# Optimization experiments

Hardware: AMD Instinct MI355X
Metric: run time of the kernel (lower is better)

## Reference

```python
import jax, jax.numpy as jnp
from jax import lax
import numpy as np

S = 3600  # spatial_size from scn.InputLayer
B = 1     # batch
P = 200000
NEG = jnp.float32(-1e30)


def setup_inputs() -> dict:
    key = jax.random.key(0)
    ks = jax.random.split(key, 10)
    coords = jax.random.randint(ks[0], (P, 2), 0, S, dtype=jnp.int32)
    features = jax.random.normal(ks[1], (P, 1), jnp.float32)
    w1 = jax.random.normal(ks[2], (5, 5, 1, 10), jnp.float32) * 0.2
    w2 = jax.random.normal(ks[3], (5, 5, 10, 64), jnp.float32) * 0.06
    w3 = jax.random.normal(ks[4], (5, 5, 64, 128), jnp.float32) * 0.025
    w4 = jax.random.normal(ks[5], (5, 5, 128, 256), jnp.float32) * 0.018
    fc1_w = jax.random.normal(ks[6], (256 * 9 * 9, 32), jnp.float32) * 0.01
    fc1_b = jax.random.normal(ks[7], (32,), jnp.float32) * 0.01
    fc2_w = jax.random.normal(ks[8], (32, 5), jnp.float32) * 0.1
    fc2_b = jax.random.normal(ks[9], (5,), jnp.float32) * 0.01
    return dict(coords=coords, features=features, w1=w1, w2=w2, w3=w3, w4=w4,
                fc1_w=fc1_w, fc1_b=fc1_b, fc2_w=fc2_w, fc2_b=fc2_b)


def _subm_conv(x, mask, w):
    # Submanifold conv == dense SAME conv on zero-filled grid, output kept
    # only at active sites (inactive inputs are exactly zero by construction).
    y = lax.conv_general_dilated(x, w, (1, 1), 'SAME',
                                 dimension_numbers=('NHWC', 'HWIO', 'NHWC'))
    return y * mask


def _sparse_maxpool(x, mask, k):
    # scn.MaxPooling: max over ACTIVE sites in each window; output site is
    # active iff any input site in the window is active, else feature = 0.
    neg = jnp.where(mask > 0, x, NEG)
    y = lax.reduce_window(neg, NEG, lax.max, (1, k, k, 1), (1, k, k, 1), 'VALID')
    new_mask = lax.reduce_window(mask, jnp.float32(0), lax.max,
                                 (1, k, k, 1), (1, k, k, 1), 'VALID')
    return jnp.where(new_mask > 0, y, 0.0), new_mask


def reference(coords, features, w1, w2, w3, w4, fc1_w, fc1_b, fc2_w, fc2_b):
    # scn.InputLayer: scatter sparse (coord, feature) pairs onto the grid
    x = jnp.zeros((B, S, S, 1), jnp.float32).at[0, coords[:, 0], coords[:, 1], :].add(features)
    mask = jnp.zeros((B, S, S, 1), jnp.float32).at[0, coords[:, 0], coords[:, 1], :].set(1.0)

    x = jax.nn.elu(_subm_conv(x, mask, w1))
    x, mask = _sparse_maxpool(x, mask, 5)   # 3600 -> 720
    x = jax.nn.elu(_subm_conv(x, mask, w2))
    x, mask = _sparse_maxpool(x, mask, 5)   # 720 -> 144
    x = jax.nn.elu(_subm_conv(x, mask, w3))
    x, mask = _sparse_maxpool(x, mask, 4)   # 144 -> 36
    x = jax.nn.elu(_subm_conv(x, mask, w4))
    x, mask = _sparse_maxpool(x, mask, 4)   # 36 -> 9

    # SparseToDense -> (B, 256, 9, 9), then view(-1, 256*9*9) in NCHW order
    h = x.transpose(0, 3, 1, 2).reshape(B, 256 * 9 * 9)
    h = jax.nn.elu(h @ fc1_w + fc1_b)
    logits = h @ fc2_w + fc2_b
    return jax.nn.softmax(logits, axis=1)
```

## Files before the change

kernel.cpp:

```cpp
#include <hip/hip_runtime.h>
#include <math.h>

#define S0 3600
#define S1 720
#define S2 144
#define S3 36
#define S4 9
#define NEGF (-1e30f)

static constexpr size_t OFF_X0  = 0;
static constexpr size_t OFF_M0B = (size_t)S0 * S0 * 4;
static constexpr size_t OFF_H1  = OFF_M0B + 1620000;
static constexpr size_t OFF_CNT = OFF_H1 + 128;
static constexpr size_t OFF_Y1H = OFF_CNT + 32;
static constexpr size_t OFF_M1  = OFF_Y1H + (size_t)S1 * S1 * 16 * 2;
static constexpr size_t OFF_M2  = 1330000;
static constexpr size_t OFF_Y3  = OFF_M2 + 20736;
static constexpr size_t OFF_M3  = OFF_Y3 + (size_t)S3 * S3 * 128 * 4;
static constexpr size_t OFF_Y4  = OFF_M3 + 1296;
static constexpr size_t OFF_Y2H = 80000000;
static constexpr size_t OFF_W2H = 84000000;
static constexpr size_t OFF_W3H = 84200000;
static constexpr size_t OFF_W4H = 84700000;

typedef __attribute__((ext_vector_type(8))) short bf16x8;
typedef __attribute__((ext_vector_type(4))) float f32x4;

__device__ __forceinline__ float eluf(float x) { return x > 0.f ? x : expm1f(x); }
__device__ __forceinline__ unsigned short f2bf(float f) {
    unsigned u = __float_as_uint(f);
    unsigned r = u + 0x7FFFu + ((u >> 16) & 1u);
    return (unsigned short)(r >> 16);
}
__device__ __forceinline__ float bf2f(unsigned short h) {
    return __uint_as_float((unsigned)h << 16);
}

__global__ __launch_bounds__(256) void k_zero(const int* __restrict__ coords,
                                              float* __restrict__ x0, int P) {
    int i = blockIdx.x * 256 + threadIdx.x;
    if (i >= P) return;
    x0[coords[2 * i] * S0 + coords[2 * i + 1]] = 0.f;
}

__global__ __launch_bounds__(256) void k_scatter(const int* __restrict__ coords,
                                                 const float* __restrict__ feats,
                                                 float* __restrict__ x0,
                                                 unsigned* __restrict__ m0b, int P) {
    int i = blockIdx.x * 256 + threadIdx.x;
    if (i >= P) return;
    int r = coords[2 * i], c = coords[2 * i + 1];
    int idx = r * S0 + c;
    atomicAdd(&x0[idx], feats[i]);
    atomicOr(&m0b[idx >> 5], 1u << (idx & 31));
}

__global__ __launch_bounds__(256) void k_l1c(const float* __restrict__ x0,
                                             const unsigned* __restrict__ m0b,
                                             const float* __restrict__ w1,
                                             const float* __restrict__ w2,
                                             const float* __restrict__ w3,
                                             const float* __restrict__ w4,
                                             unsigned short* __restrict__ y1h,
                                             unsigned char* __restrict__ m1,
                                             unsigned short* __restrict__ w2h,
                                             unsigned short* __restrict__ w3h,
                                             unsigned short* __restrict__ w4h) {
    int b = blockIdx.x;
    int tid = threadIdx.x;
    if (b >= 2025) {
        int blk = b - 2025;
        if (blk < 13) {
            int t = blk * 256 + tid;
            int s = t >> 8, rem = t & 255;
            int nt = rem >> 6, lane = rem & 63;
            int quad = lane >> 4, n = lane & 15;
            int tap = 2 * s + (quad >> 1);
#pragma unroll
            for (int j = 0; j < 8; j++) {
                int ci = (quad & 1) * 8 + j;
                float v = 0.f;
                if (tap < 25 && ci < 10) v = w2[(tap * 10 + ci) * 64 + nt * 16 + n];
                w2h[(size_t)t * 8 + j] = f2bf(v);
            }
        } else if (blk < 113) {
            int t = (blk - 13) * 256 + tid;
            int s = t >> 9, rem = t & 511;
            int nt = rem >> 6, lane = rem & 63;
            int quad = lane >> 4, n = lane & 15;
            int t5 = s >> 1, cib = s & 1;
#pragma unroll
            for (int j = 0; j < 8; j++) {
                int ci = cib * 32 + quad * 8 + j;
                float v = w3[(size_t)(t5 * 64 + ci) * 128 + nt * 16 + n];
                w3h[(size_t)t * 8 + j] = f2bf(v);
            }
        } else {
            int t = (blk - 113) * 256 + tid;
            int s = t >> 10, rem = t & 1023;
            int nt = rem >> 6, lane = rem & 63;
            int quad = lane >> 4, n = lane & 15;
            int t5 = s >> 2, cib = s & 3;
#pragma unroll
            for (int j = 0; j < 8; j++) {
                int ci = cib * 32 + quad * 8 + j;
                float v = w4[(size_t)(t5 * 128 + ci) * 256 + nt * 16 + n];
                w4h[(size_t)t * 8 + j] = f2bf(v);
            }
        }
        return;
    }
    __shared__ float w1s[250];
    if (tid < 250) w1s[tid] = w1[tid];
    __syncthreads();
    int t = b * 256 + tid;
    int pr = t / S1, pc = t % S1;
    int r0 = pr * 5 - 2, c0 = pc * 5 - 2;
    unsigned rows[9];
#pragma unroll
    for (int rr = 0; rr < 9; rr++) {
        unsigned bits = 0;
        int gr = r0 + rr;
        if (gr >= 0 && gr < S0) {
            int cs = c0 < 0 ? 0 : c0;
            int ce = c0 + 8 > S0 - 1 ? S0 - 1 : c0 + 8;
            int span = ce - cs;
            size_t i0 = (size_t)gr * S0 + cs;
            unsigned sh = (unsigned)(i0 & 31);
            unsigned long long two = (unsigned long long)m0b[i0 >> 5] >> sh;
            if ((int)sh + span >= 32)
                two |= (unsigned long long)m0b[(i0 >> 5) + 1] << (32 - sh);
            bits = (unsigned)(two & ((1u << (span + 1)) - 1));
            bits <<= (cs - c0);
        }
        rows[rr] = bits;
    }
    unsigned any25 = 0;
#pragma unroll
    for (int dy = 0; dy < 5; dy++) any25 |= (rows[2 + dy] >> 2) & 0x1Fu;
    uint4* yo = (uint4*)&y1h[(size_t)t * 16];
    if (!any25) {
        yo[0] = make_uint4(0, 0, 0, 0);
        yo[1] = make_uint4(0, 0, 0, 0);
        m1[t] = 0;
        return;
    }
    float2 mx[5];
#pragma unroll
    for (int q = 0; q < 5; q++) mx[q] = make_float2(NEGF, NEGF);
    for (int dy = 0; dy < 5; dy++) {
        unsigned crow = (rows[2 + dy] >> 2) & 0x1Fu;
        while (crow) {
            int dx = __ffs(crow) - 1; crow &= crow - 1;
            float2 acc[5];
#pragma unroll
            for (int q = 0; q < 5; q++) acc[q] = make_float2(0.f, 0.f);
#pragma unroll
            for (int ky = 0; ky < 5; ky++) {
                unsigned nrow = (rows[dy + ky] >> dx) & 0x1Fu;
                size_t rowbase = (size_t)(r0 + dy + ky) * S0 + (c0 + dx);
                while (nrow) {
                    int kx = __ffs(nrow) - 1; nrow &= nrow - 1;
                    float xv = x0[rowbase + kx];
                    const float2* wp = (const float2*)&w1s[(ky * 5 + kx) * 10];
#pragma unroll
                    for (int q = 0; q < 5; q++) {
                        float2 w = wp[q];
                        acc[q].x = fmaf(xv, w.x, acc[q].x);
                        acc[q].y = fmaf(xv, w.y, acc[q].y);
                    }
                }
            }
#pragma unroll
            for (int q = 0; q < 5; q++) {
                mx[q].x = fmaxf(mx[q].x, acc[q].x);
                mx[q].y = fmaxf(mx[q].y, acc[q].y);
            }
        }
    }
    unsigned u[8];
#pragma unroll
    for (int q = 0; q < 5; q++) {
        unsigned short h0 = f2bf(eluf(mx[q].x));
        unsigned short h1 = f2bf(eluf(mx[q].y));
        u[q] = (unsigned)h0 | ((unsigned)h1 << 16);
    }
    u[5] = 0; u[6] = 0; u[7] = 0;
    yo[0] = make_uint4(u[0], u[1], u[2], u[3]);
    yo[1] = make_uint4(u[4], u[5], u[6], u[7]);
    m1[t] = 1;
}

__global__ __launch_bounds__(256, 4) void k_l2(const unsigned short* __restrict__ y1h,
                                               const unsigned char* __restrict__ m1,
                                               const unsigned short* __restrict__ w2h,
                                               unsigned short* __restrict__ y2h,
                                               unsigned char* __restrict__ m2) {
    __shared__ unsigned short winh[240 * 24];
    __shared__ unsigned char sm[196];
    int b = blockIdx.x;
    int bpr = b / 72, bpc = b % 72;
    int r0 = bpr * 10 - 2, c0 = bpc * 10 - 2;
    int tid = threadIdx.x;
    if (tid < 240) {
        uint4 v0 = make_uint4(0, 0, 0, 0), v1 = v0;
        if (tid < 196) {
            int gr = r0 + tid / 14, gc = c0 + tid % 14;
            bool ok = (gr >= 0 && gr < S1 && gc >= 0 && gc < S1);
            sm[tid] = ok ? m1[gr * S1 + gc] : (unsigned char)0;
            if (ok) {
                const uint4* src = (const uint4*)&y1h[(size_t)(gr * S1 + gc) * 16];
                v0 = src[0];
                v1 = src[1];
            }
        }
        uint4* dh = (uint4*)&winh[tid * 24];
        dh[0] = v0;
        dh[1] = v1;
    }
    __syncthreads();
    int wv = tid >> 6;
    int a = wv >> 1, bq = wv & 1;
    int lane = tid & 63, quad = lane >> 4, n = lane & 15;
    int cql = lane & 31, s01l = lane >> 5;
    bool pv = false;
    if (cql < 25)
        pv = sm[(a * 5 + 2 + cql / 5) * 14 + s01l * 5 + 2 + cql % 5] != 0;
    unsigned long long bal = __ballot(pv);
    unsigned mb[2];
    mb[0] = (unsigned)(bal & 0x1FFFFFFull);
    mb[1] = (unsigned)((bal >> 32) & 0x1FFFFFFull);
    const bf16x8* wh8 = (const bf16x8*)w2h;
    const bf16x8* xh8 = (const bf16x8*)winh;
    int oct = quad & 1, qh = quad >> 1;
    int base[2][2];
#pragma unroll
    for (int s01 = 0; s01 < 2; s01++)
#pragma unroll
        for (int mt = 0; mt < 2; mt++) {
            int cell = mt * 16 + n;
            base[s01][mt] = ((a * 5 + cell / 5) * 14 + s01 * 5 + cell % 5) * 3 + oct;
        }
    constexpr int TOFF[26] = {0, 1, 2, 3, 4, 14, 15, 16, 17, 18, 28, 29, 30, 31,
                              32, 42, 43, 44, 45, 46, 56, 57, 58, 59, 60, 70};
    f32x4 acc[2][2][2];
#pragma unroll
    for (int s01 = 0; s01 < 2; s01++)
#pragma unroll
        for (int mt = 0; mt < 2; mt++)
#pragma unroll
            for (int ntl = 0; ntl < 2; ntl++) acc[s01][mt][ntl] = (f32x4){0.f, 0.f, 0.f, 0.f};
#pragma unroll
    for (int s = 0; s < 13; s++) {
        int toff3 = 3 * (qh ? TOFF[2 * s + 1] : TOFF[2 * s]);
        bf16x8 ah[2][2];
#pragma unroll
        for (int s01 = 0; s01 < 2; s01++)
#pragma unroll
            for (int mt = 0; mt < 2; mt++) ah[s01][mt] = xh8[base[s01][mt] + toff3];
#pragma unroll
        for (int ntl = 0; ntl < 2; ntl++) {
            bf16x8 bh = wh8[(s * 4 + bq * 2 + ntl) * 64 + lane];
#pragma unroll
            for (int s01 = 0; s01 < 2; s01++)
#pragma unroll
                for (int mt = 0; mt < 2; mt++)
                    acc[s01][mt][ntl] = __builtin_amdgcn_mfma_f32_16x16x32_bf16(ah[s01][mt], bh, acc[s01][mt][ntl], 0, 0, 0);
        }
    }
#pragma unroll
    for (int s01 = 0; s01 < 2; s01++) {
        int gsite = (bpr * 2 + a) * S2 + bpc * 2 + s01;
#pragma unroll
        for (int ntl = 0; ntl < 2; ntl++) {
            float m = NEGF;
#pragma unroll
            for (int mt = 0; mt < 2; mt++) {
#pragma unroll
                for (int r = 0; r < 4; r++) {
                    int cell = mt * 16 + quad * 4 + r;
                    if (cell < 25 && (mb[s01] & (1u << cell))) m = fmaxf(m, acc[s01][mt][ntl][r]);
                }
            }
            m = fmaxf(m, __shfl_xor(m, 16, 64));
            m = fmaxf(m, __shfl_xor(m, 32, 64));
            if (quad == 0) {
                int nt = bq * 2 + ntl;
                y2h[(size_t)gsite * 64 + nt * 16 + n] = mb[s01] ? f2bf(eluf(m)) : (unsigned short)0;
            }
        }
        if (bq == 0 && lane == 0) m2[gsite] = mb[s01] ? 1 : 0;
    }
}

__global__ __launch_bounds__(256) void k_l3(const unsigned short* __restrict__ y2h,
                                            const unsigned char* __restrict__ m2,
                                            const unsigned short* __restrict__ w3h,
                                            float* __restrict__ y3,
                                            unsigned char* __restrict__ m3) {
    __shared__ uint4 win_h4[144 * 9];
    __shared__ unsigned char sm[64];
    int b = blockIdx.x;
    int pr2 = b / 18, pc2 = b % 18;
    int r0 = pr2 * 8 - 2, c0 = pc2 * 8 - 2;
    int tid = threadIdx.x;
    for (int k = tid; k < 1152; k += 256) {
        int cellk = k >> 3, q = k & 7;
        int gr = r0 + cellk / 12, gc = c0 + cellk % 12;
        uint4 vh = make_uint4(0, 0, 0, 0);
        if (gr >= 0 && gr < S2 && gc >= 0 && gc < S2)
            vh = ((const uint4*)y2h)[(size_t)(gr * S2 + gc) * 8 + q];
        win_h4[cellk * 9 + q] = vh;
    }
    if (tid < 64) sm[tid] = m2[(pr2 * 8 + (tid >> 3)) * S2 + pc2 * 8 + (tid & 7)];
    __syncthreads();
    const bf16x8* winh8 = (const bf16x8*)win_h4;
    const bf16x8* w3h8 = (const bf16x8*)w3h;
    int wv = tid >> 6, lane = tid & 63;
    int quad = lane >> 4, n = lane & 15;
    int cellr = n >> 2, cellc = n & 3;
    f32x4 acc[4][2];
#pragma unroll
    for (int si = 0; si < 4; si++)
#pragma unroll
        for (int ntl = 0; ntl < 2; ntl++) acc[si][ntl] = (f32x4){0.f, 0.f, 0.f, 0.f};
    int bb = (wv * 2) * 64 + lane;
    bf16x8 bh0 = w3h8[bb];
    bf16x8 bh1 = w3h8[bb + 64];
#pragma unroll 2
    for (int s = 0; s < 50; s++) {
        int sp = s + 1 < 50 ? s + 1 : 0;
        int nb = (sp * 8 + wv * 2) * 64 + lane;
        bf16x8 nh0 = w3h8[nb];
        bf16x8 nh1 = w3h8[nb + 64];
        int t5 = s >> 1, cib = s & 1;
        int ky = t5 / 5, kx = t5 % 5;
        int common = ((cellr + ky) * 12 + (cellc + kx)) * 9 + cib * 4 + quad;
#pragma unroll
        for (int si = 0; si < 4; si++) {
            bf16x8 ah = winh8[common + (si >> 1) * 432 + (si & 1) * 36];
            acc[si][0] = __builtin_amdgcn_mfma_f32_16x16x32_bf16(ah, bh0, acc[si][0], 0, 0, 0);
            acc[si][1] = __builtin_amdgcn_mfma_f32_16x16x32_bf16(ah, bh1, acc[si][1], 0, 0, 0);
        }
        bh0 = nh0; bh1 = nh1;
    }
#pragma unroll
    for (int si = 0; si < 4; si++) {
        int srb = (si >> 1) * 4, scb = (si & 1) * 4;
        bool anyv = false;
#pragma unroll
        for (int i = 0; i < 16; i++) anyv |= (sm[(srb + (i >> 2)) * 8 + scb + (i & 3)] != 0);
        int sg = (2 * pr2 + (si >> 1)) * S3 + 2 * pc2 + (si & 1);
#pragma unroll
        for (int ntl = 0; ntl < 2; ntl++) {
            float mv = NEGF;
#pragma unroll
            for (int r = 0; r < 4; r++) {
                int cell = quad * 4 + r;
                if (sm[(srb + (cell >> 2)) * 8 + scb + (cell & 3)]) mv = fmaxf(mv, acc[si][ntl][r]);
            }
            mv = fmaxf(mv, __shfl_xor(mv, 16, 64));
            mv = fmaxf(mv, __shfl_xor(mv, 32, 64));
            if (quad == 0)
                y3[(size_t)sg * 128 + (wv * 2 + ntl) * 16 + n] = anyv ? eluf(mv) : 0.f;
        }
        if (tid == 0) m3[sg] = anyv ? 1 : 0;
    }
}

__global__ __launch_bounds__(1024) void k_l4(const float* __restrict__ y3,
                                             const unsigned char* __restrict__ m3,
                                             const unsigned short* __restrict__ w4h,
                                             float* __restrict__ y4) {
    __shared__ unsigned short winh[1120 * 8];
    __shared__ unsigned char sm[16];
    int p = blockIdx.x;
    int ppr = p / S4, ppc = p % S4;
    int r0 = ppr * 4 - 2, c0 = ppc * 4 - 2;
    int tid = threadIdx.x;
    for (int k = tid; k < 2048; k += 1024) {
        int cellk = k >> 5, q = k & 31;
        int cr = cellk >> 3, cc = cellk & 7;
        int gr = r0 + cr, gc = c0 + cc;
        float4 v = make_float4(0.f, 0.f, 0.f, 0.f);
        if (gr >= 0 && gr < S3 && gc >= 0 && gc < S3)
            v = ((const float4*)y3)[((size_t)gr * S3 + gc) * 32 + q];
        unsigned short h0 = f2bf(v.x), h1 = f2bf(v.y), h2 = f2bf(v.z), h3 = f2bf(v.w);
        unsigned uh0 = (unsigned)h0 | ((unsigned)h1 << 16);
        unsigned uh1 = (unsigned)h2 | ((unsigned)h3 << 16);
        ((uint2*)winh)[cr * 280 + cc * 34 + q] = make_uint2(uh0, uh1);
    }
    if (tid < 16) sm[tid] = m3[(ppr * 4 + (tid >> 2)) * S3 + ppc * 4 + (tid & 3)];
    __syncthreads();
    const bf16x8* winh8 = (const bf16x8*)winh;
    const bf16x8* w4h8 = (const bf16x8*)w4h;
    int wv = tid >> 6, lane = tid & 63;
    int quad = lane >> 4, n = lane & 15;
    int cellr = n >> 2, cellc = n & 3;
    f32x4 acc = {0.f, 0.f, 0.f, 0.f};
    int wb = wv * 64 + lane;
    bf16x8 bha = w4h8[wb];
    bf16x8 bhb = w4h8[1024 + wb];
#pragma unroll 2
    for (int s = 0; s < 100; s++) {
        int sp = s + 2 < 100 ? s + 2 : 0;
        bf16x8 nh = w4h8[sp * 1024 + wb];
        int t5 = s >> 2, cib = s & 3;
        int ky = t5 / 5, kx = t5 % 5;
        int aidx = (cellr + ky) * 140 + (cellc + kx) * 17 + cib * 4 + quad;
        bf16x8 ah = winh8[aidx];
        acc = __builtin_amdgcn_mfma_f32_16x16x32_bf16(ah, bha, acc, 0, 0, 0);
        bha = bhb; bhb = nh;
    }
    bool anyv = false;
#pragma unroll
    for (int i = 0; i < 16; i++) anyv |= (sm[i] != 0);
    float m = NEGF;
#pragma unroll
    for (int r = 0; r < 4; r++) {
        int cell = quad * 4 + r;
        if (sm[cell]) m = fmaxf(m, acc[r]);
    }
    m = fmaxf(m, __shfl_xor(m, 16, 64));
    m = fmaxf(m, __shfl_xor(m, 32, 64));
    if (quad == 0)
        y4[(size_t)p * 256 + wv * 16 + n] = anyv ? eluf(m) : 0.f;
}

__global__ __launch_bounds__(256) void k_fc(const float* __restrict__ y4,
                                            const float* __restrict__ fc1_w,
                                            const float* __restrict__ fc1_b,
                                            const float* __restrict__ fc2_w,
                                            const float* __restrict__ fc2_b,
                                            float* __restrict__ h1,
                                            unsigned* __restrict__ cnt,
                                            float* __restrict__ out) {
    __shared__ float wsum[4][32];
    __shared__ int lastflag;
    __shared__ float hv[32];
    __shared__ float lg[5];
    int t = threadIdx.x;
    int i = blockIdx.x * 256 + t;
    int c = i / 81, rem = i % 81;
    float x = y4[(size_t)rem * 256 + c];
    const float4* wr = (const float4*)&fc1_w[(size_t)i * 32];
    float4 w[8];
#pragma unroll
    for (int q = 0; q < 8; q++) w[q] = wr[q];
    int lane = t & 63, wv = t >> 6;
#pragma unroll
    for (int q = 0; q < 8; q++) {
#pragma unroll
        for (int k = 0; k < 4; k++) {
            float v = x * ((&w[q].x)[k]);
            v += __shfl_down(v, 32, 64);
            v += __shfl_down(v, 16, 64);
            v += __shfl_down(v, 8, 64);
            v += __shfl_down(v, 4, 64);
            v += __shfl_down(v, 2, 64);
            v += __shfl_down(v, 1, 64);
            if (lane == 0) wsum[wv][q * 4 + k] = v;
        }
    }
    __syncthreads();
    if (t < 32) {
        float s = wsum[0][t] + wsum[1][t] + wsum[2][t] + wsum[3][t];
        atomicAdd(&h1[t], s);
    }
    __threadfence();
    __syncthreads();
    if (t == 0) lastflag = (atomicAdd(cnt, 1u) == 80u) ? 1 : 0;
    __syncthreads();
    if (!lastflag) return;
    if (t < 32) hv[t] = eluf(atomicAdd(&h1[t], 0.f) + fc1_b[t]);
    __syncthreads();
    if (t < 5) {
        float s = fc2_b[t];
        for (int j = 0; j < 32; j++) s = fmaf(hv[j], fc2_w[j * 5 + t], s);
        lg[t] = s;
    }
    __syncthreads();
    if (t == 0) {
        float m = lg[0];
        for (int k = 1; k < 5; k++) m = fmaxf(m, lg[k]);
        float e[5], sum = 0.f;
        for (int k = 0; k < 5; k++) { e[k] = expf(lg[k] - m); sum += e[k]; }
        for (int k = 0; k < 5; k++) out[k] = e[k] / sum;
    }
}

extern "C" void kernel_launch(void* const* d_in, const int* in_sizes, int n_in,
                              void* d_out, int out_size, void* d_ws, size_t ws_size,
                              hipStream_t stream) {
    const int* coords = (const int*)d_in[0];
    const float* feats = (const float*)d_in[1];
    const float* w1 = (const float*)d_in[2];
    const float* w2 = (const float*)d_in[3];
    const float* w3 = (const float*)d_in[4];
    const float* w4 = (const float*)d_in[5];
    const float* fc1w = (const float*)d_in[6];
    const float* fc1b = (const float*)d_in[7];
    const float* fc2w = (const float*)d_in[8];
    const float* fc2b = (const float*)d_in[9];
    float* out = (float*)d_out;
    char* ws = (char*)d_ws;
    float* x0 = (float*)(ws + OFF_X0);
    unsigned* m0b = (unsigned*)(ws + OFF_M0B);
    unsigned short* y1h = (unsigned short*)(ws + OFF_Y1H);
    unsigned char* m1g = (unsigned char*)(ws + OFF_M1);
    unsigned char* m2g = (unsigned char*)(ws + OFF_M2);
    float* y3 = (float*)(ws + OFF_Y3);
    unsigned char* m3g = (unsigned char*)(ws + OFF_M3);
    float* y4 = (float*)(ws + OFF_Y4);
    float* h1 = (float*)(ws + OFF_H1);
    unsigned* cnt = (unsigned*)(ws + OFF_CNT);
    unsigned short* y2h = (unsigned short*)(ws + OFF_Y2H);
    unsigned short* w2h = (unsigned short*)(ws + OFF_W2H);
    unsigned short* w3h = (unsigned short*)(ws + OFF_W3H);
    unsigned short* w4h = (unsigned short*)(ws + OFF_W4H);
    int P = in_sizes[1];

    hipMemsetAsync(ws + OFF_M0B, 0, 1620000 + 160, stream);
    k_zero<<<(P + 255) / 256, 256, 0, stream>>>(coords, x0, P);
    k_scatter<<<(P + 255) / 256, 256, 0, stream>>>(coords, feats, x0, m0b, P);
    k_l1c<<<2025 + 513, 256, 0, stream>>>(x0, m0b, w1, w2, w3, w4,
                                          y1h, m1g, w2h, w3h, w4h);
    k_l2<<<72 * 72, 256, 0, stream>>>(y1h, m1g, w2h, y2h, m2g);
    k_l3<<<18 * 18, 256, 0, stream>>>(y2h, m2g, w3h, y3, m3g);
    k_l4<<<S4 * S4, 1024, 0, stream>>>(y3, m3g, w4h, y4);
    k_fc<<<81, 256, 0, stream>>>(y4, fc1w, fc1b, fc2w, fc2b, h1, cnt, out);
}
```

Before: 227.2 us.

## Widen layer-2 tiles to four pooled columns and skip inactive y1 stores

Each layer-2 block now covers a 2x4 group of pooled output sites, loading a 14x24 halo window instead of 14x14. Weight fragment loads are reused across twice as many MFMAs and halo overhead per output drops. Layer 1 no longer writes zeros for inactive sites; layer 2 only reads y1 where the mask is set and zero-fills otherwise. In exchange, accumulator register count doubles, the occupancy hint drops to 2, and the grid halves.

```diff
diff --git a/kernel.cpp b/kernel.cpp
--- a/kernel.cpp
+++ b/kernel.cpp
@@ -138,10 +138,7 @@
     unsigned any25 = 0;
 #pragma unroll
     for (int dy = 0; dy < 5; dy++) any25 |= (rows[2 + dy] >> 2) & 0x1Fu;
-    uint4* yo = (uint4*)&y1h[(size_t)t * 16];
     if (!any25) {
-        yo[0] = make_uint4(0, 0, 0, 0);
-        yo[1] = make_uint4(0, 0, 0, 0);
         m1[t] = 0;
         return;
     }
@@ -186,35 +183,36 @@
         u[q] = (unsigned)h0 | ((unsigned)h1 << 16);
     }
     u[5] = 0; u[6] = 0; u[7] = 0;
+    uint4* yo = (uint4*)&y1h[(size_t)t * 16];
     yo[0] = make_uint4(u[0], u[1], u[2], u[3]);
     yo[1] = make_uint4(u[4], u[5], u[6], u[7]);
     m1[t] = 1;
 }
 
-__global__ __launch_bounds__(256, 4) void k_l2(const unsigned short* __restrict__ y1h,
+__global__ __launch_bounds__(256, 2) void k_l2(const unsigned short* __restrict__ y1h,
                                                const unsigned char* __restrict__ m1,
                                                const unsigned short* __restrict__ w2h,
                                                unsigned short* __restrict__ y2h,
                                                unsigned char* __restrict__ m2) {
-    __shared__ unsigned short winh[240 * 24];
-    __shared__ unsigned char sm[196];
+    __shared__ unsigned short winh[408 * 24];
+    __shared__ unsigned char sm[336];
     int b = blockIdx.x;
-    int bpr = b / 72, bpc = b % 72;
-    int r0 = bpr * 10 - 2, c0 = bpc * 10 - 2;
+    int bpr = b / 36, bpc = b % 36;
+    int r0 = bpr * 10 - 2, c0 = bpc * 20 - 2;
     int tid = threadIdx.x;
-    if (tid < 240) {
+    for (int k = tid; k < 336; k += 256) {
+        int hr = k / 24, hc = k % 24;
+        int gr = r0 + hr, gc = c0 + hc;
+        bool ok = (gr >= 0 && gr < S1 && gc >= 0 && gc < S1);
+        unsigned char msk = ok ? m1[gr * S1 + gc] : (unsigned char)0;
+        sm[k] = msk;
         uint4 v0 = make_uint4(0, 0, 0, 0), v1 = v0;
-        if (tid < 196) {
-            int gr = r0 + tid / 14, gc = c0 + tid % 14;
-            bool ok = (gr >= 0 && gr < S1 && gc >= 0 && gc < S1);
-            sm[tid] = ok ? m1[gr * S1 + gc] : (unsigned char)0;
-            if (ok) {
-                const uint4* src = (const uint4*)&y1h[(size_t)(gr * S1 + gc) * 16];
-                v0 = src[0];
-                v1 = src[1];
-            }
-        }
-        uint4* dh = (uint4*)&winh[tid * 24];
+        if (msk) {
+            const uint4* src = (const uint4*)&y1h[(size_t)(gr * S1 + gc) * 16];
+            v0 = src[0];
+            v1 = src[1];
+        }
+        uint4* dh = (uint4*)&winh[k * 24];
         dh[0] = v0;
         dh[1] = v1;
     }
@@ -222,55 +220,59 @@
     int wv = tid >> 6;
     int a = wv >> 1, bq = wv & 1;
     int lane = tid & 63, quad = lane >> 4, n = lane & 15;
-    int cql = lane & 31, s01l = lane >> 5;
-    bool pv = false;
-    if (cql < 25)
-        pv = sm[(a * 5 + 2 + cql / 5) * 14 + s01l * 5 + 2 + cql % 5] != 0;
-    unsigned long long bal = __ballot(pv);
-    unsigned mb[2];
-    mb[0] = (unsigned)(bal & 0x1FFFFFFull);
-    mb[1] = (unsigned)((bal >> 32) & 0x1FFFFFFull);
+    int cql = lane & 31, scl = lane >> 5;
+    unsigned mb[4];
+#pragma unroll
+    for (int g = 0; g < 2; g++) {
+        bool pv = false;
+        int sc = g * 2 + scl;
+        if (cql < 25)
+            pv = sm[(a * 5 + 2 + cql / 5) * 24 + sc * 5 + 2 + cql % 5] != 0;
+        unsigned long long bal = __ballot(pv);
+        mb[g * 2] = (unsigned)(bal & 0x1FFFFFFull);
+        mb[g * 2 + 1] = (unsigned)((bal >> 32) & 0x1FFFFFFull);
+    }
     const bf16x8* wh8 = (const bf16x8*)w2h;
     const bf16x8* xh8 = (const bf16x8*)winh;
     int oct = quad & 1, qh = quad >> 1;
-    int base[2][2];
-#pragma unroll
-    for (int s01 = 0; s01 < 2; s01++)
+    int base[4][2];
+#pragma unroll
+    for (int sc = 0; sc < 4; sc++)
 #pragma unroll
         for (int mt = 0; mt < 2; mt++) {
             int cell = mt * 16 + n;
-            base[s01][mt] = ((a * 5 + cell / 5) * 14 + s01 * 5 + cell % 5) * 3 + oct;
-        }
-    constexpr int TOFF[26] = {0, 1, 2, 3, 4, 14, 15, 16, 17, 18, 28, 29, 30, 31,
-                              32, 42, 43, 44, 45, 46, 56, 57, 58, 59, 60, 70};
-    f32x4 acc[2][2][2];
-#pragma unroll
-    for (int s01 = 0; s01 < 2; s01++)
+            base[sc][mt] = ((a * 5 + cell / 5) * 24 + sc * 5 + cell % 5) * 3 + oct;
+        }
+    constexpr int TOFF24[26] = {0, 1, 2, 3, 4, 24, 25, 26, 27, 28, 48, 49, 50, 51,
+                                52, 72, 73, 74, 75, 76, 96, 97, 98, 99, 100, 120};
+    f32x4 acc[4][2][2];
+#pragma unroll
+    for (int sc = 0; sc < 4; sc++)
 #pragma unroll
         for (int mt = 0; mt < 2; mt++)
 #pragma unroll
-            for (int ntl = 0; ntl < 2; ntl++) acc[s01][mt][ntl] = (f32x4){0.f, 0.f, 0.f, 0.f};
+            for (int ntl = 0; ntl < 2; ntl++) acc[sc][mt][ntl] = (f32x4){0.f, 0.f, 0.f, 0.f};
 #pragma unroll
     for (int s = 0; s < 13; s++) {
-        int toff3 = 3 * (qh ? TOFF[2 * s + 1] : TOFF[2 * s]);
-        bf16x8 ah[2][2];
-#pragma unroll
-        for (int s01 = 0; s01 < 2; s01++)
-#pragma unroll
-            for (int mt = 0; mt < 2; mt++) ah[s01][mt] = xh8[base[s01][mt] + toff3];
+        int toff3 = 3 * (qh ? TOFF24[2 * s + 1] : TOFF24[2 * s]);
+        bf16x8 ah[4][2];
+#pragma unroll
+        for (int sc = 0; sc < 4; sc++)
+#pragma unroll
+            for (int mt = 0; mt < 2; mt++) ah[sc][mt] = xh8[base[sc][mt] + toff3];
 #pragma unroll
         for (int ntl = 0; ntl < 2; ntl++) {
             bf16x8 bh = wh8[(s * 4 + bq * 2 + ntl) * 64 + lane];
 #pragma unroll
-            for (int s01 = 0; s01 < 2; s01++)
+            for (int sc = 0; sc < 4; sc++)
 #pragma unroll
                 for (int mt = 0; mt < 2; mt++)
-                    acc[s01][mt][ntl] = __builtin_amdgcn_mfma_f32_16x16x32_bf16(ah[s01][mt], bh, acc[s01][mt][ntl], 0, 0, 0);
-        }
-    }
-#pragma unroll
-    for (int s01 = 0; s01 < 2; s01++) {
-        int gsite = (bpr * 2 + a) * S2 + bpc * 2 + s01;
+                    acc[sc][mt][ntl] = __builtin_amdgcn_mfma_f32_16x16x32_bf16(ah[sc][mt], bh, acc[sc][mt][ntl], 0, 0, 0);
+        }
+    }
+#pragma unroll
+    for (int sc = 0; sc < 4; sc++) {
+        int gsite = (bpr * 2 + a) * S2 + bpc * 4 + sc;
 #pragma unroll
         for (int ntl = 0; ntl < 2; ntl++) {
             float m = NEGF;
@@ -279,17 +281,17 @@
 #pragma unroll
                 for (int r = 0; r < 4; r++) {
                     int cell = mt * 16 + quad * 4 + r;
-                    if (cell < 25 && (mb[s01] & (1u << cell))) m = fmaxf(m, acc[s01][mt][ntl][r]);
+                    if (cell < 25 && (mb[sc] & (1u << cell))) m = fmaxf(m, acc[sc][mt][ntl][r]);
                 }
             }
             m = fmaxf(m, __shfl_xor(m, 16, 64));
             m = fmaxf(m, __shfl_xor(m, 32, 64));
             if (quad == 0) {
                 int nt = bq * 2 + ntl;
-                y2h[(size_t)gsite * 64 + nt * 16 + n] = mb[s01] ? f2bf(eluf(m)) : (unsigned short)0;
-            }
-        }
-        if (bq == 0 && lane == 0) m2[gsite] = mb[s01] ? 1 : 0;
+                y2h[(size_t)gsite * 64 + nt * 16 + n] = mb[sc] ? f2bf(eluf(m)) : (unsigned short)0;
+            }
+        }
+        if (bq == 0 && lane == 0) m2[gsite] = mb[sc] ? 1 : 0;
     }
 }
 
@@ -525,7 +527,7 @@
     k_scatter<<<(P + 255) / 256, 256, 0, stream>>>(coords, feats, x0, m0b, P);
     k_l1c<<<2025 + 513, 256, 0, stream>>>(x0, m0b, w1, w2, w3, w4,
                                           y1h, m1g, w2h, w3h, w4h);
-    k_l2<<<72 * 72, 256, 0, stream>>>(y1h, m1g, w2h, y2h, m2g);
+    k_l2<<<72 * 36, 256, 0, stream>>>(y1h, m1g, w2h, y2h, m2g);
     k_l3<<<18 * 18, 256, 0, stream>>>(y2h, m2g, w3h, y3, m3g);
     k_l4<<<S4 * S4, 1024, 0, stream>>>(y3, m3g, w4h, y4);
     k_fc<<<81, 256, 0, stream>>>(y4, fc1w, fc1b, fc2w, fc2b, h1, cnt, out);
```

Result: slower. 239.8 us (+5.6%).
